# Performance work log

Hardware: AMD Instinct MI355X
Metric: run time of the kernel (lower is better)

Reference implementation:

```python
import jax, jax.numpy as jnp
import numpy as np

N_NODES = 100000
N_EDGES = 1600000
IN_DIM = 128
HID = 256
N_CLS = 32
BN_EPS = 1e-5


def _sage_conv(x, src, dst, Wl, bl, Wr, n_nodes):
    # PyG SAGEConv (mean aggr): out = lin_l(mean_{j->i} x_j) + lin_r(x_i)
    msgs = x[src]                                              # [E, D] gather
    agg = jax.ops.segment_sum(msgs, dst, num_segments=n_nodes)  # [N, D]
    deg = jax.ops.segment_sum(jnp.ones((src.shape[0],), x.dtype), dst,
                              num_segments=n_nodes)
    agg = agg / jnp.maximum(deg, 1.0)[:, None]                 # mean
    return agg @ Wl + bl + x @ Wr


def _batch_norm(x, gamma, beta):
    mu = jnp.mean(x, axis=0)
    var = jnp.var(x, axis=0)
    return (x - mu) * jax.lax.rsqrt(var + BN_EPS) * gamma + beta


def setup_inputs() -> dict:
    key = jax.random.key(0)
    ks = jax.random.split(key, 8)
    s = lambda d: 1.0 / np.sqrt(d)
    return {
        "x": jax.random.normal(ks[0], (N_NODES, IN_DIM), jnp.float32),
        "edge_src": jax.random.randint(ks[1], (N_EDGES,), 0, N_NODES),
        "edge_dst": jax.random.randint(ks[2], (N_EDGES,), 0, N_NODES),
        "W1l": jax.random.normal(ks[3], (IN_DIM, HID), jnp.float32) * s(IN_DIM),
        "b1": jnp.zeros((HID,), jnp.float32),
        "W1r": jax.random.normal(ks[4], (IN_DIM, HID), jnp.float32) * s(IN_DIM),
        "g1": jnp.ones((HID,), jnp.float32),
        "be1": jnp.zeros((HID,), jnp.float32),
        "W2l": jax.random.normal(ks[5], (HID, HID), jnp.float32) * s(HID),
        "b2": jnp.zeros((HID,), jnp.float32),
        "W2r": jax.random.normal(ks[6], (HID, HID), jnp.float32) * s(HID),
        "g2": jnp.ones((HID,), jnp.float32),
        "be2": jnp.zeros((HID,), jnp.float32),
        "Wfc": jax.random.normal(ks[7], (HID, N_CLS), jnp.float32) * s(HID),
        "bfc": jnp.zeros((N_CLS,), jnp.float32),
    }


def reference(x, edge_src, edge_dst, W1l, b1, W1r, g1, be1,
              W2l, b2, W2r, g2, be2, Wfc, bfc):
    n = x.shape[0]
    h = _sage_conv(x, edge_src, edge_dst, W1l, b1, W1r, n)
    h = jax.nn.relu(_batch_norm(h, g1, be1))
    # dropout is identity in deterministic/eval mode
    h = _sage_conv(h, edge_src, edge_dst, W2l, b2, W2r, n)
    h = jax.nn.relu(_batch_norm(h, g2, be2))
    return h @ Wfc + bfc
```

## Files before the change

### kernel.cpp

```cpp
#include <hip/hip_runtime.h>

#define N_NODES 100000
#define N_EDGES 1600000
#define IN_DIM 128
#define HID 256
#define N_CLS 32
#define BN_EPS 1e-5f

#define SCAN_CHUNK 1024
#define SCAN_NB ((N_NODES + SCAN_CHUNK - 1) / SCAN_CHUNK)
#define GEMM_NBY ((N_NODES + 127) / 128)
#define GEMM_NB (GEMM_NBY * 2)

#define NBUCK 16
#define BUCK_NODES 6250
#define BUCK_CAP 112000
#define PASSA_CHUNK 4096
#define PASSA_NB ((N_EDGES + PASSA_CHUNK - 1) / PASSA_CHUNK)
#define FILL_SUBS 64

typedef unsigned short bf16;
typedef __attribute__((ext_vector_type(8))) short short8;
typedef __attribute__((ext_vector_type(4))) float float4v;
typedef __attribute__((ext_vector_type(2))) float floatx2;

__device__ __forceinline__ float bf2f(bf16 h) {
    return __uint_as_float(((unsigned int)h) << 16);
}
__device__ __forceinline__ bf16 f2bf(float f) {
    unsigned int u = __float_as_uint(f);
    u += 0x7FFFu + ((u >> 16) & 1u);
    return (bf16)(u >> 16);
}
__device__ __forceinline__ float blo(unsigned int u) { return __uint_as_float(u << 16); }
__device__ __forceinline__ float bhi(unsigned int u) { return __uint_as_float(u & 0xFFFF0000u); }
__device__ __forceinline__ unsigned int pack2(float lo, float hi) {
    return (unsigned int)f2bf(lo) | ((unsigned int)f2bf(hi) << 16);
}

__device__ __forceinline__ void acc8_fp8(uint2 w, float* a) {
    floatx2 f0 = __builtin_amdgcn_cvt_pk_f32_fp8(w.x, false);
    floatx2 f1 = __builtin_amdgcn_cvt_pk_f32_fp8(w.x, true);
    floatx2 f2 = __builtin_amdgcn_cvt_pk_f32_fp8(w.y, false);
    floatx2 f3 = __builtin_amdgcn_cvt_pk_f32_fp8(w.y, true);
    a[0] += f0.x; a[1] += f0.y; a[2] += f1.x; a[3] += f1.y;
    a[4] += f2.x; a[5] += f2.y; a[6] += f3.x; a[7] += f3.y;
}
__device__ __forceinline__ unsigned int pack4_fp8(float a, float b, float c, float d) {
    int p = 0;
    p = __builtin_amdgcn_cvt_pk_fp8_f32(a, b, p, false);
    p = __builtin_amdgcn_cvt_pk_fp8_f32(c, d, p, true);
    return (unsigned int)p;
}

__device__ __forceinline__ void gload16(const void* g, void* l) {
    __builtin_amdgcn_global_load_lds(
        (const __attribute__((address_space(1))) void*)g,
        (__attribute__((address_space(3))) void*)l, 16, 0, 0);
}


__global__ __launch_bounds__(256) void bucket_scatter_kernel(
    const int* __restrict__ esrc, const int* __restrict__ edst,
    int* __restrict__ counts, int* __restrict__ bcur, int2* __restrict__ bstore) {
    __shared__ int lhist[NBUCK], lbase[NBUCK], gbase[NBUCK], lcur[NBUCK];
    __shared__ int2 stage[PASSA_CHUNK];
    const int tid = threadIdx.x;
    if (tid < NBUCK) lhist[tid] = 0;
    __syncthreads();

    const int base = blockIdx.x * PASSA_CHUNK;
    const int nedge = min(PASSA_CHUNK, N_EDGES - base);
    const bool act = (tid * 16) < nedge;
    int s[16], d[16], bk[16];
    if (act) {
        const int4* s4 = (const int4*)(esrc + base + tid * 16);
        const int4* d4 = (const int4*)(edst + base + tid * 16);
#pragma unroll
        for (int t = 0; t < 4; ++t) {
            int4 sv = s4[t], dv = d4[t];
            s[t * 4 + 0] = sv.x; s[t * 4 + 1] = sv.y; s[t * 4 + 2] = sv.z; s[t * 4 + 3] = sv.w;
            d[t * 4 + 0] = dv.x; d[t * 4 + 1] = dv.y; d[t * 4 + 2] = dv.z; d[t * 4 + 3] = dv.w;
        }
#pragma unroll
        for (int u = 0; u < 16; ++u) {
            bk[u] = (int)((unsigned)d[u] / BUCK_NODES);
            atomicAdd(&counts[d[u]], 1);
            atomicAdd(&lhist[bk[u]], 1);
        }
    }
    __syncthreads();
    if (tid == 0) {
        int run = 0;
#pragma unroll
        for (int b = 0; b < NBUCK; ++b) { lbase[b] = run; lcur[b] = run; run += lhist[b]; }
    }
    if (tid < NBUCK) gbase[tid] = atomicAdd(&bcur[tid], lhist[tid]);
    __syncthreads();
    if (act) {
#pragma unroll
        for (int u = 0; u < 16; ++u) {
            int p = atomicAdd(&lcur[bk[u]], 1);
            stage[p] = make_int2(s[u], d[u]);
        }
    }
    __syncthreads();
    for (int p = tid; p < nedge; p += 256) {
        int2 e = stage[p];
        int b = (int)((unsigned)e.y / BUCK_NODES);
        int gp = gbase[b] + (p - lbase[b]);
        if (gp < BUCK_CAP) bstore[(size_t)b * BUCK_CAP + gp] = e;
    }
}


__global__ __launch_bounds__(256) void fill_bucket_kernel(
    const int2* __restrict__ bstore, const int* __restrict__ bcnt,
    const int* __restrict__ off, int* __restrict__ cursor, int* __restrict__ csr) {
    const int bk = blockIdx.x & (NBUCK - 1);
    const int sub = blockIdx.x >> 4;
    const int n = bcnt[bk];
    const int2* ep = bstore + (size_t)bk * BUCK_CAP;
    for (int i = sub * 256 + threadIdx.x; i < n; i += 256 * FILL_SUBS) {
        int2 e = ep[i];
        int p = atomicAdd(&cursor[e.y], 1);
        csr[off[e.y] + p] = e.x;
    }
}


__global__ void scan1_kernel(const int* __restrict__ counts, int* __restrict__ bsums) {
    __shared__ int wsum[4];
    int base = blockIdx.x * SCAN_CHUNK + threadIdx.x * 4;
    int s = 0;
    if (base + 4 <= N_NODES) {
        int4 v = *(const int4*)(counts + base);
        s = v.x + v.y + v.z + v.w;
    } else {
        for (int j = 0; j < 4; ++j) if (base + j < N_NODES) s += counts[base + j];
    }
    for (int d = 32; d > 0; d >>= 1) s += __shfl_down(s, d, 64);
    if ((threadIdx.x & 63) == 0) wsum[threadIdx.x >> 6] = s;
    __syncthreads();
    if (threadIdx.x == 0) bsums[blockIdx.x] = wsum[0] + wsum[1] + wsum[2] + wsum[3];
}

__global__ void scan2_kernel(const int* __restrict__ bsums, int* __restrict__ boffs) {
    __shared__ int sh[128];
    int i = threadIdx.x;
    int v = (i < SCAN_NB) ? bsums[i] : 0;
    sh[i] = v;
    __syncthreads();
    for (int d = 1; d < 128; d <<= 1) {
        int t = (i >= d) ? sh[i - d] : 0;
        __syncthreads();
        sh[i] += t;
        __syncthreads();
    }
    if (i < SCAN_NB) boffs[i] = sh[i] - v;
}

__global__ void scan3_kernel(const int* __restrict__ counts, const int* __restrict__ boffs,
                             int* __restrict__ off) {
    __shared__ int sh[256];
    int tid = threadIdx.x;
    int base = blockIdx.x * SCAN_CHUNK + tid * 4;
    int c0 = 0, c1 = 0, c2 = 0, c3 = 0;
    if (base + 4 <= N_NODES) {
        int4 v = *(const int4*)(counts + base);
        c0 = v.x; c1 = v.y; c2 = v.z; c3 = v.w;
    } else {
        if (base + 0 < N_NODES) c0 = counts[base + 0];
        if (base + 1 < N_NODES) c1 = counts[base + 1];
        if (base + 2 < N_NODES) c2 = counts[base + 2];
        if (base + 3 < N_NODES) c3 = counts[base + 3];
    }
    int ts = c0 + c1 + c2 + c3;
    sh[tid] = ts;
    __syncthreads();
    for (int d = 1; d < 256; d <<= 1) {
        int t = (tid >= d) ? sh[tid - d] : 0;
        __syncthreads();
        sh[tid] += t;
        __syncthreads();
    }
    int run = boffs[blockIdx.x] + sh[tid] - ts;
    if (base + 0 < N_NODES) off[base + 0] = run; run += c0;
    if (base + 1 < N_NODES) off[base + 1] = run; run += c1;
    if (base + 2 < N_NODES) off[base + 2] = run; run += c2;
    if (base + 3 < N_NODES) off[base + 3] = run;
    if (blockIdx.x == 0 && tid == 0) off[N_NODES] = N_EDGES;
}


__global__ void convert_x_kernel(const float* __restrict__ x, bf16* __restrict__ xb,
                                 unsigned char* __restrict__ xf8) {
    int i = blockIdx.x * blockDim.x + threadIdx.x;
    int total4 = N_NODES * IN_DIM / 4;
    if (i >= total4) return;
    float4 v = ((const float4*)x)[i];
    ushort4 r;
    r.x = f2bf(v.x); r.y = f2bf(v.y); r.z = f2bf(v.z); r.w = f2bf(v.w);
    ((ushort4*)xb)[i] = r;
    ((unsigned int*)xf8)[i] = pack4_fp8(v.x, v.y, v.z, v.w);
}


__global__ void prep_weights_kernel(const float* __restrict__ W1l, const float* __restrict__ W1r,
                                    const float* __restrict__ W2l, const float* __restrict__ W2r,
                                    const float* __restrict__ Wfc,
                                    bf16* __restrict__ w1lt, bf16* __restrict__ w1rt,
                                    bf16* __restrict__ w2lt, bf16* __restrict__ w2rt,
                                    bf16* __restrict__ wfct) {
    const int S1 = IN_DIM * HID;
    const int S2 = HID * HID;
    const int S3 = HID * N_CLS;
    int i = blockIdx.x * blockDim.x + threadIdx.x;
    if (i < 2 * S1 + 2 * S2) {
        const float* W; bf16* Wt; int K, idx;
        if (i < S1)          { W = W1l; Wt = w1lt; K = IN_DIM; idx = i; }
        else if (i < 2 * S1) { W = W1r; Wt = w1rt; K = IN_DIM; idx = i - S1; }
        else if (i < 2 * S1 + S2) { W = W2l; Wt = w2lt; K = HID; idx = i - 2 * S1; }
        else                 { W = W2r; Wt = w2rt; K = HID; idx = i - 2 * S1 - S2; }
        int k = idx / HID, n = idx - k * HID;
        Wt[(size_t)n * K + k] = f2bf(W[idx]);
    } else if (i < 2 * S1 + 2 * S2 + S3) {
        int idx = i - 2 * S1 - 2 * S2;
        int k = idx >> 5, n = idx & 31;
        wfct[(size_t)n * HID + k] = f2bf(Wfc[idx]);
    }
}


__global__ void aggregate1_kernel(const unsigned char* __restrict__ xf8, const int* __restrict__ off,
                                  const int* __restrict__ csr, bf16* __restrict__ out) {
    int t = blockIdx.x * blockDim.x + threadIdx.x;
    int node = t >> 4;
    int sl = t & 15;
    if (node >= N_NODES) return;
    int s = off[node], e = off[node + 1];
    float inv = 1.0f / (float)max(e - s, 1);
    const uint2* f = (const uint2*)xf8;
    float a[8] = {0.f, 0.f, 0.f, 0.f, 0.f, 0.f, 0.f, 0.f};
    int i = s;
    for (; i + 4 <= e; i += 4) {
        int u0 = csr[i], u1 = csr[i + 1], u2 = csr[i + 2], u3 = csr[i + 3];
        uint2 w0 = f[(size_t)u0 * 16 + sl];
        uint2 w1 = f[(size_t)u1 * 16 + sl];
        uint2 w2 = f[(size_t)u2 * 16 + sl];
        uint2 w3 = f[(size_t)u3 * 16 + sl];
        acc8_fp8(w0, a); acc8_fp8(w1, a); acc8_fp8(w2, a); acc8_fp8(w3, a);
    }
    for (; i < e; ++i) {
        uint2 w = f[(size_t)csr[i] * 16 + sl];
        acc8_fp8(w, a);
    }
    uint4 r;
    r.x = pack2(a[0] * inv, a[1] * inv);
    r.y = pack2(a[2] * inv, a[3] * inv);
    r.z = pack2(a[4] * inv, a[5] * inv);
    r.w = pack2(a[6] * inv, a[7] * inv);
    ((uint4*)out)[(size_t)node * 16 + sl] = r;
}

__global__ void aggregate2_kernel(const unsigned char* __restrict__ hf8, const int* __restrict__ off,
                                  const int* __restrict__ csr, bf16* __restrict__ out) {
    int t = blockIdx.x * blockDim.x + threadIdx.x;
    int node = t >> 5;
    int sl = t & 31;
    if (node >= N_NODES) return;
    int s = off[node], e = off[node + 1];
    float inv = 1.0f / (float)max(e - s, 1);
    const uint2* f = (const uint2*)hf8;
    float a[8] = {0.f, 0.f, 0.f, 0.f, 0.f, 0.f, 0.f, 0.f};
    int i = s;
    for (; i + 4 <= e; i += 4) {
        int u0 = csr[i], u1 = csr[i + 1], u2 = csr[i + 2], u3 = csr[i + 3];
        uint2 w0 = f[(size_t)u0 * 32 + sl];
        uint2 w1 = f[(size_t)u1 * 32 + sl];
        uint2 w2 = f[(size_t)u2 * 32 + sl];
        uint2 w3 = f[(size_t)u3 * 32 + sl];
        acc8_fp8(w0, a); acc8_fp8(w1, a); acc8_fp8(w2, a); acc8_fp8(w3, a);
    }
    for (; i < e; ++i) {
        uint2 w = f[(size_t)csr[i] * 32 + sl];
        acc8_fp8(w, a);
    }
    uint4 r;
    r.x = pack2(a[0] * inv, a[1] * inv);
    r.y = pack2(a[2] * inv, a[3] * inv);
    r.z = pack2(a[4] * inv, a[5] * inv);
    r.w = pack2(a[6] * inv, a[7] * inv);
    ((uint4*)out)[(size_t)node * 32 + sl] = r;
}


#define AT_SZ 4096

__device__ __forceinline__ void stage_tile(
    const bf16* __restrict__ Ap, const bf16* __restrict__ Wp, int K, int k0,
    int tile_m, int tile_n, int M, int wave, int lane,
    bf16* bufA, bf16* bufW) {
#pragma unroll
    for (int is = 0; is < 2; ++is) {
        int lin = (wave * 2 + is) * 1024 + lane * 16;
        int row = lin >> 6;
        int seg = (lin >> 4) & 3;
        int ga = min(tile_m + row, M - 1);
        gload16(Ap + (size_t)ga * K + k0 + seg * 8, (char*)bufA + (wave * 2 + is) * 1024);
        gload16(Wp + (size_t)(tile_n + row) * K + k0 + seg * 8, (char*)bufW + (wave * 2 + is) * 1024);
    }
}

__global__ __launch_bounds__(256) void gemm_dual_mfma(
    const bf16* __restrict__ A, const bf16* __restrict__ WtA, int KA,
    const bf16* __restrict__ Bm, const bf16* __restrict__ WtB, int KB,
    const float* __restrict__ bias, bf16* __restrict__ C, int M,
    float* __restrict__ psum, float* __restrict__ psq) {
    __shared__ bf16 As[3 * AT_SZ];
    __shared__ bf16 Ws[3 * AT_SZ];
    __shared__ float sred[4][64];
    __shared__ float qred[4][64];
    const int tid = threadIdx.x;
    const int lane = tid & 63;
    const int wave = tid >> 6;
    const int rw = (wave >> 1) * 64;
    const int cw = (wave & 1) * 64;
    const int lrow = lane & 15;
    const int quad = lane >> 4;
    const int tile_m = blockIdx.y * 128;
    const int tile_n = blockIdx.x * 128;

    float4v acc[4][4];
#pragma unroll
    for (int i = 0; i < 4; ++i)
#pragma unroll
        for (int j = 0; j < 4; ++j) acc[i][j] = (float4v){0.f, 0.f, 0.f, 0.f};

    const int NTA = KA >> 5;
    const int NT = NTA + (KB >> 5);
    auto tsrc = [&](int t, const bf16*& Ap, const bf16*& Wp, int& K, int& k0) {
        if (t < NTA) { Ap = A;  Wp = WtA; K = KA; k0 = t << 5; }
        else         { Ap = Bm; Wp = WtB; K = KB; k0 = (t - NTA) << 5; }
    };

#pragma unroll
    for (int t = 0; t < 2; ++t) {
        const bf16 *Ap, *Wp; int K, k0; tsrc(t, Ap, Wp, K, k0);
        stage_tile(Ap, Wp, K, k0, tile_m, tile_n, M, wave, lane,
                   As + t * AT_SZ, Ws + t * AT_SZ);
    }

    for (int t = 0; t < NT; ++t) {
        if (t + 2 < NT) {
            const bf16 *Ap, *Wp; int K, k0; tsrc(t + 2, Ap, Wp, K, k0);
            int b = (t + 2) % 3;
            stage_tile(Ap, Wp, K, k0, tile_m, tile_n, M, wave, lane,
                       As + b * AT_SZ, Ws + b * AT_SZ);
        }
        if (t + 2 < NT)      asm volatile("s_waitcnt vmcnt(8)" ::: "memory");
        else if (t + 1 < NT) asm volatile("s_waitcnt vmcnt(4)" ::: "memory");
        else                 asm volatile("s_waitcnt vmcnt(0)" ::: "memory");
        __builtin_amdgcn_s_barrier();
        asm volatile("" ::: "memory");

        const bf16* bA = As + (t % 3) * AT_SZ;
        const bf16* bW = Ws + (t % 3) * AT_SZ;
        short8 a[4], b[4];
#pragma unroll
        for (int i = 0; i < 4; ++i)
            a[i] = *(const short8*)(bA + (rw + i * 16 + lrow) * 32 + quad * 8);
#pragma unroll
        for (int j = 0; j < 4; ++j)
            b[j] = *(const short8*)(bW + (cw + j * 16 + lrow) * 32 + quad * 8);
#pragma unroll
        for (int i = 0; i < 4; ++i)
#pragma unroll
            for (int j = 0; j < 4; ++j)
                acc[i][j] = __builtin_amdgcn_mfma_f32_16x16x32_bf16(a[i], b[j], acc[i][j], 0, 0, 0);

        asm volatile("" ::: "memory");
        __builtin_amdgcn_s_barrier();
    }

    bf16* slice = As + wave * 1024;
    float bvj[4];
#pragma unroll
    for (int j = 0; j < 4; ++j) bvj[j] = bias[tile_n + cw + j * 16 + lrow];
    float cs[4] = {0.f, 0.f, 0.f, 0.f}, cq[4] = {0.f, 0.f, 0.f, 0.f};

#pragma unroll
    for (int i = 0; i < 4; ++i) {
#pragma unroll
        for (int j = 0; j < 4; ++j) {
#pragma unroll
            for (int r = 0; r < 4; ++r) {
                int row = tile_m + rw + i * 16 + quad * 4 + r;
                float v = acc[i][j][r] + bvj[j];
                if (row < M) { cs[j] += v; cq[j] += v * v; }
                slice[(quad * 4 + r) * 64 + ((j ^ quad) * 16) + lrow] = f2bf(v);
            }
        }
        __syncthreads();
#pragma unroll
        for (int c = 0; c < 2; ++c) {
            int ch = lane + c * 64;
            int lr = ch >> 3, sg = ch & 7;
            int grow = tile_m + rw + i * 16 + lr;
            if (grow < M) {
                const bf16* srcp = slice + lr * 64 + (((sg >> 1) ^ (lr >> 2)) << 4) + ((sg & 1) << 3);
                uint4 v = *(const uint4*)srcp;
                *(uint4*)(C + (size_t)grow * HID + tile_n + cw + sg * 8) = v;
            }
        }
        __syncthreads();
    }

#pragma unroll
    for (int j = 0; j < 4; ++j) {
        cs[j] += __shfl_xor(cs[j], 16, 64); cs[j] += __shfl_xor(cs[j], 32, 64);
        cq[j] += __shfl_xor(cq[j], 16, 64); cq[j] += __shfl_xor(cq[j], 32, 64);
    }
    if (quad == 0) {
#pragma unroll
        for (int j = 0; j < 4; ++j) {
            sred[wave][j * 16 + lrow] = cs[j];
            qred[wave][j * 16 + lrow] = cq[j];
        }
    }
    __syncthreads();
    int bid = blockIdx.y * gridDim.x + blockIdx.x;
    if (tid < 128) {
        int grp = tid >> 6, idx = tid & 63;
        psum[(size_t)bid * 128 + tid] = sred[grp][idx] + sred[grp + 2][idx];
    } else {
        int t = tid - 128;
        int grp = t >> 6, idx = t & 63;
        psq[(size_t)bid * 128 + t] = qred[grp][idx] + qred[grp + 2][idx];
    }
}

__global__ void bn_finalize_kernel(const float* __restrict__ psum, const float* __restrict__ psq,
                                   float* __restrict__ stats, int nby) {
    const float* src = blockIdx.y ? psq : psum;
    int c = threadIdx.x;
    int bx = c >> 7, cl = c & 127;
    int per = (nby + gridDim.x - 1) / gridDim.x;
    int b0 = blockIdx.x * per, b1 = min(b0 + per, nby);
    float s = 0.f;
    for (int by = b0; by < b1; ++by) s += src[(size_t)(by * 2 + bx) * 128 + cl];
    atomicAdd(&stats[blockIdx.y * HID + c], s);
}


__global__ void bn_apply_relu_kernel(bf16* __restrict__ h, unsigned char* __restrict__ hf8,
                                     const float* __restrict__ stats,
                                     const float* __restrict__ g, const float* __restrict__ be,
                                     int M) {
    int i4 = blockIdx.x * blockDim.x + threadIdx.x;
    int total4 = M * (HID / 4);
    if (i4 >= total4) return;
    int col4 = i4 & (HID / 4 - 1);
    ushort4 v = ((const ushort4*)h)[i4];
    float invN = 1.0f / (float)M;
    float o[4] = {bf2f(v.x), bf2f(v.y), bf2f(v.z), bf2f(v.w)};
#pragma unroll
    for (int j = 0; j < 4; ++j) {
        int col = col4 * 4 + j;
        float mu = stats[col] * invN;
        float var = stats[HID + col] * invN - mu * mu;
        float sc = rsqrtf(var + BN_EPS) * g[col];
        float val = (o[j] - mu) * sc + be[col];
        o[j] = val > 0.f ? val : 0.f;
    }
    ushort4 r;
    r.x = f2bf(o[0]); r.y = f2bf(o[1]); r.z = f2bf(o[2]); r.w = f2bf(o[3]);
    ((ushort4*)h)[i4] = r;
    ((unsigned int*)hf8)[i4] = pack4_fp8(o[0], o[1], o[2], o[3]);
}


#define BSTR 264

__global__ __launch_bounds__(256) void fc_bn_mfma_kernel(
    const bf16* __restrict__ h, const float* __restrict__ stats,
    const float* __restrict__ g, const float* __restrict__ be,
    const bf16* __restrict__ WfcT, const float* __restrict__ bfc,
    float* __restrict__ out, int M) {
    __shared__ bf16 Bs[32 * BSTR];
    __shared__ float sc_s[HID], sh_s[HID];
    int tid = threadIdx.x;
    for (int i = tid; i < 32 * 32; i += 256) {
        int rrow = i >> 5, seg = i & 31;
        *(uint4*)(Bs + rrow * BSTR + seg * 8) = *(const uint4*)(WfcT + (size_t)rrow * HID + seg * 8);
    }
    {
        float invN = 1.0f / (float)M;
        float mu = stats[tid] * invN;
        float var = stats[HID + tid] * invN - mu * mu;
        float s = rsqrtf(var + BN_EPS) * g[tid];
        sc_s[tid] = s;
        sh_s[tid] = be[tid] - mu * s;
    }
    __syncthreads();
    int wave = tid >> 6, lane = tid & 63, lrow = lane & 15, quad = lane >> 4;
    int row = blockIdx.x * 64 + wave * 16 + lrow;
    const bf16* hrow = h + (size_t)row * HID;
    float4v acc0 = {0.f, 0.f, 0.f, 0.f}, acc1 = {0.f, 0.f, 0.f, 0.f};
#pragma unroll
    for (int ks = 0; ks < 8; ++ks) {
        int k0 = ks * 32 + quad * 8;
        uint4 av = {0u, 0u, 0u, 0u};
        if (row < M) av = *(const uint4*)(hrow + k0);
        union { unsigned int u[4]; short8 s8; } cvt;
        unsigned int* avp = (unsigned int*)&av;
#pragma unroll
        for (int t = 0; t < 4; ++t) {
            int k = k0 + t * 2;
            float v0 = blo(avp[t]) * sc_s[k] + sh_s[k];
            float v1 = bhi(avp[t]) * sc_s[k + 1] + sh_s[k + 1];
            v0 = v0 > 0.f ? v0 : 0.f;
            v1 = v1 > 0.f ? v1 : 0.f;
            cvt.u[t] = pack2(v0, v1);
        }
        short8 b0 = *(const short8*)(Bs + lrow * BSTR + k0);
        short8 b1 = *(const short8*)(Bs + (16 + lrow) * BSTR + k0);
        acc0 = __builtin_amdgcn_mfma_f32_16x16x32_bf16(cvt.s8, b0, acc0, 0, 0, 0);
        acc1 = __builtin_amdgcn_mfma_f32_16x16x32_bf16(cvt.s8, b1, acc1, 0, 0, 0);
    }
    int orow = blockIdx.x * 64 + wave * 16 + quad * 4;
    float bv0 = bfc[lrow], bv1 = bfc[16 + lrow];
#pragma unroll
    for (int r = 0; r < 4; ++r) {
        int rr = orow + r;
        if (rr < M) {
            out[(size_t)rr * N_CLS + lrow] = acc0[r] + bv0;
            out[(size_t)rr * N_CLS + 16 + lrow] = acc1[r] + bv1;
        }
    }
}


extern "C" void kernel_launch(void* const* d_in, const int* in_sizes, int n_in,
                              void* d_out, int out_size, void* d_ws, size_t ws_size,
                              hipStream_t stream) {
    const float* x   = (const float*)d_in[0];
    const int* esrc  = (const int*)d_in[1];
    const int* edst  = (const int*)d_in[2];
    const float* W1l = (const float*)d_in[3];
    const float* b1  = (const float*)d_in[4];
    const float* W1r = (const float*)d_in[5];
    const float* g1  = (const float*)d_in[6];
    const float* be1 = (const float*)d_in[7];
    const float* W2l = (const float*)d_in[8];
    const float* b2  = (const float*)d_in[9];
    const float* W2r = (const float*)d_in[10];
    const float* g2  = (const float*)d_in[11];
    const float* be2 = (const float*)d_in[12];
    const float* Wfc = (const float*)d_in[13];
    const float* bfc = (const float*)d_in[14];
    float* out = (float*)d_out;

    char* ws = (char*)d_ws;
    size_t o = 0;
    auto carve = [&](size_t bytes) {
        char* p = ws + o;
        o = (o + bytes + 255) & ~(size_t)255;
        return p;
    };
    int*   off    = (int*)carve((N_NODES + 1) * sizeof(int));
    int*   cursor = (int*)carve(N_NODES * sizeof(int));
    int*   csr    = (int*)carve(N_EDGES * sizeof(int));
    int*   bsums  = (int*)carve(SCAN_NB * sizeof(int));
    int*   boffs  = (int*)carve(SCAN_NB * sizeof(int));
    int*   bcur   = (int*)carve(NBUCK * sizeof(int));
    float* stats1 = (float*)carve(2 * HID * sizeof(float));
    float* stats2 = (float*)carve(2 * HID * sizeof(float));
    float* psum   = (float*)carve((size_t)GEMM_NB * 128 * sizeof(float));
    float* psq    = (float*)carve((size_t)GEMM_NB * 128 * sizeof(float));
    bf16*  w1lt   = (bf16*)carve((size_t)IN_DIM * HID * sizeof(bf16));
    bf16*  w1rt   = (bf16*)carve((size_t)IN_DIM * HID * sizeof(bf16));
    bf16*  w2lt   = (bf16*)carve((size_t)HID * HID * sizeof(bf16));
    bf16*  w2rt   = (bf16*)carve((size_t)HID * HID * sizeof(bf16));
    bf16*  wfct   = (bf16*)carve((size_t)N_CLS * HID * sizeof(bf16));
    bf16*  agg    = (bf16*)carve((size_t)N_NODES * HID * sizeof(bf16));
    bf16*  h1     = (bf16*)carve((size_t)N_NODES * HID * sizeof(bf16));
    bf16*  h2     = (bf16*)carve((size_t)N_NODES * HID * sizeof(bf16));
    bf16*          xb   = h2;
    unsigned char* xf8  = (unsigned char*)h2 + (size_t)N_NODES * IN_DIM * sizeof(bf16);
    unsigned char* h1f8 = (unsigned char*)h2;
    int2*          bstore = (int2*)agg;

    if (o > ws_size) return;

    hipMemsetAsync(cursor, 0, N_NODES * sizeof(int), stream);
    hipMemsetAsync(bcur, 0, NBUCK * sizeof(int), stream);
    hipMemsetAsync(stats1, 0, 2 * HID * sizeof(float), stream);
    hipMemsetAsync(stats2, 0, 2 * HID * sizeof(float), stream);

    bucket_scatter_kernel<<<PASSA_NB, 256, 0, stream>>>(esrc, edst, cursor, bcur, bstore);
    scan1_kernel<<<SCAN_NB, 256, 0, stream>>>(cursor, bsums);
    scan2_kernel<<<1, 128, 0, stream>>>(bsums, boffs);
    scan3_kernel<<<SCAN_NB, 256, 0, stream>>>(cursor, boffs, off);
    hipMemsetAsync(cursor, 0, N_NODES * sizeof(int), stream);
    fill_bucket_kernel<<<NBUCK * FILL_SUBS, 256, 0, stream>>>(bstore, bcur, off, cursor, csr);

    convert_x_kernel<<<(N_NODES * IN_DIM / 4 + 255) / 256, 256, 0, stream>>>(x, xb, xf8);
    {
        int total = 2 * IN_DIM * HID + 2 * HID * HID + HID * N_CLS;
        prep_weights_kernel<<<(total + 255) / 256, 256, 0, stream>>>(
            W1l, W1r, W2l, W2r, Wfc, w1lt, w1rt, w2lt, w2rt, wfct);
    }

    const dim3 ggrid(HID / 128, GEMM_NBY);

    aggregate1_kernel<<<(N_NODES * 16 + 255) / 256, 256, 0, stream>>>(xf8, off, csr, agg);
    gemm_dual_mfma<<<ggrid, 256, 0, stream>>>(
        agg, w1lt, IN_DIM, xb, w1rt, IN_DIM, b1, h1, N_NODES, psum, psq);
    bn_finalize_kernel<<<dim3(8, 2), 256, 0, stream>>>(psum, psq, stats1, GEMM_NBY);
    {
        int total4 = N_NODES * (HID / 4);
        bn_apply_relu_kernel<<<(total4 + 255) / 256, 256, 0, stream>>>(h1, h1f8, stats1, g1, be1, N_NODES);
    }

    aggregate2_kernel<<<(N_NODES * 32 + 255) / 256, 256, 0, stream>>>(h1f8, off, csr, agg);
    gemm_dual_mfma<<<ggrid, 256, 0, stream>>>(
        agg, w2lt, HID, h1, w2rt, HID, b2, h2, N_NODES, psum, psq);
    bn_finalize_kernel<<<dim3(8, 2), 256, 0, stream>>>(psum, psq, stats2, GEMM_NBY);

    fc_bn_mfma_kernel<<<(N_NODES + 63) / 64, 256, 0, stream>>>(
        h2, stats2, g2, be2, wfct, bfc, out, N_NODES);
}
```

Measured before the change: 557.2 us.

## Replace global per-node degree atomics with LDS bucket histograms

The per-edge global atomicAdd on node degree counts is removed from the bucket scatter pass. A new kernel builds per-bucket degree histograms in shared memory over slices of each bucket, and writes partial counts that the first scan kernel sums into the final counts. The scatter chunk size is also halved to launch more blocks. This trades 1.6M scattered global atomics for an extra kernel launch plus about 6.4 MB of partial-count writes and reads.

```diff
diff --git a/kernel.cpp b/kernel.cpp
--- a/kernel.cpp
+++ b/kernel.cpp
@@ -15,9 +15,10 @@
 #define NBUCK 16
 #define BUCK_NODES 6250
 #define BUCK_CAP 112000
-#define PASSA_CHUNK 4096
+#define PASSA_CHUNK 2048
 #define PASSA_NB ((N_EDGES + PASSA_CHUNK - 1) / PASSA_CHUNK)
 #define FILL_SUBS 64
+#define HSUBS 16
 
 typedef unsigned short bf16;
 typedef __attribute__((ext_vector_type(8))) short short8;
@@ -62,7 +63,7 @@
 
 __global__ __launch_bounds__(256) void bucket_scatter_kernel(
     const int* __restrict__ esrc, const int* __restrict__ edst,
-    int* __restrict__ counts, int* __restrict__ bcur, int2* __restrict__ bstore) {
+    int* __restrict__ bcur, int2* __restrict__ bstore) {
     __shared__ int lhist[NBUCK], lbase[NBUCK], gbase[NBUCK], lcur[NBUCK];
     __shared__ int2 stage[PASSA_CHUNK];
     const int tid = threadIdx.x;
@@ -71,21 +72,20 @@
 
     const int base = blockIdx.x * PASSA_CHUNK;
     const int nedge = min(PASSA_CHUNK, N_EDGES - base);
-    const bool act = (tid * 16) < nedge;
-    int s[16], d[16], bk[16];
+    const bool act = (tid * 8) < nedge;
+    int s[8], d[8], bk[8];
     if (act) {
-        const int4* s4 = (const int4*)(esrc + base + tid * 16);
-        const int4* d4 = (const int4*)(edst + base + tid * 16);
-#pragma unroll
-        for (int t = 0; t < 4; ++t) {
+        const int4* s4 = (const int4*)(esrc + base + tid * 8);
+        const int4* d4 = (const int4*)(edst + base + tid * 8);
+#pragma unroll
+        for (int t = 0; t < 2; ++t) {
             int4 sv = s4[t], dv = d4[t];
             s[t * 4 + 0] = sv.x; s[t * 4 + 1] = sv.y; s[t * 4 + 2] = sv.z; s[t * 4 + 3] = sv.w;
             d[t * 4 + 0] = dv.x; d[t * 4 + 1] = dv.y; d[t * 4 + 2] = dv.z; d[t * 4 + 3] = dv.w;
         }
 #pragma unroll
-        for (int u = 0; u < 16; ++u) {
+        for (int u = 0; u < 8; ++u) {
             bk[u] = (int)((unsigned)d[u] / BUCK_NODES);
-            atomicAdd(&counts[d[u]], 1);
             atomicAdd(&lhist[bk[u]], 1);
         }
     }
@@ -99,7 +99,7 @@
     __syncthreads();
     if (act) {
 #pragma unroll
-        for (int u = 0; u < 16; ++u) {
+        for (int u = 0; u < 8; ++u) {
             int p = atomicAdd(&lcur[bk[u]], 1);
             stage[p] = make_int2(s[u], d[u]);
         }
@@ -111,6 +111,28 @@
         int gp = gbase[b] + (p - lbase[b]);
         if (gp < BUCK_CAP) bstore[(size_t)b * BUCK_CAP + gp] = e;
     }
+}
+
+
+__global__ __launch_bounds__(256) void bucket_hist_kernel(
+    const int2* __restrict__ bstore, const int* __restrict__ bcnt,
+    int* __restrict__ partial) {
+    __shared__ int hist[BUCK_NODES];
+    const int bk = blockIdx.x & (NBUCK - 1);
+    const int sl = blockIdx.x >> 4;
+    for (int i = threadIdx.x; i < BUCK_NODES; i += 256) hist[i] = 0;
+    __syncthreads();
+    const int n = bcnt[bk];
+    const int per = (n + HSUBS - 1) / HSUBS;
+    const int i0 = sl * per, i1 = min(i0 + per, n);
+    const int2* ep = bstore + (size_t)bk * BUCK_CAP;
+    const int nbase = bk * BUCK_NODES;
+    for (int i = i0 + threadIdx.x; i < i1; i += 256) {
+        atomicAdd(&hist[ep[i].y - nbase], 1);
+    }
+    __syncthreads();
+    int* dst = partial + (size_t)sl * N_NODES + nbase;
+    for (int i = threadIdx.x; i < BUCK_NODES; i += 256) dst[i] = hist[i];
 }
 
 
@@ -129,16 +151,30 @@
 }
 
 
-__global__ void scan1_kernel(const int* __restrict__ counts, int* __restrict__ bsums) {
+__global__ void scan1_kernel(const int* __restrict__ partial, int* __restrict__ counts,
+                             int* __restrict__ bsums) {
     __shared__ int wsum[4];
     int base = blockIdx.x * SCAN_CHUNK + threadIdx.x * 4;
-    int s = 0;
+    int c0 = 0, c1 = 0, c2 = 0, c3 = 0;
     if (base + 4 <= N_NODES) {
-        int4 v = *(const int4*)(counts + base);
-        s = v.x + v.y + v.z + v.w;
+#pragma unroll
+        for (int sl = 0; sl < HSUBS; ++sl) {
+            int4 v = *(const int4*)(partial + (size_t)sl * N_NODES + base);
+            c0 += v.x; c1 += v.y; c2 += v.z; c3 += v.w;
+        }
+        int4 w; w.x = c0; w.y = c1; w.z = c2; w.w = c3;
+        *(int4*)(counts + base) = w;
     } else {
-        for (int j = 0; j < 4; ++j) if (base + j < N_NODES) s += counts[base + j];
-    }
+        for (int j = 0; j < 4; ++j) {
+            if (base + j < N_NODES) {
+                int c = 0;
+                for (int sl = 0; sl < HSUBS; ++sl) c += partial[(size_t)sl * N_NODES + base + j];
+                counts[base + j] = c;
+                if (j == 0) c0 = c; else if (j == 1) c1 = c; else if (j == 2) c2 = c; else c3 = c;
+            }
+        }
+    }
+    int s = c0 + c1 + c2 + c3;
     for (int d = 32; d > 0; d >>= 1) s += __shfl_down(s, d, 64);
     if ((threadIdx.x & 63) == 0) wsum[threadIdx.x >> 6] = s;
     __syncthreads();
@@ -590,16 +626,17 @@
     unsigned char* xf8  = (unsigned char*)h2 + (size_t)N_NODES * IN_DIM * sizeof(bf16);
     unsigned char* h1f8 = (unsigned char*)h2;
     int2*          bstore = (int2*)agg;
+    int*           partial = (int*)h1;
 
     if (o > ws_size) return;
 
-    hipMemsetAsync(cursor, 0, N_NODES * sizeof(int), stream);
     hipMemsetAsync(bcur, 0, NBUCK * sizeof(int), stream);
     hipMemsetAsync(stats1, 0, 2 * HID * sizeof(float), stream);
     hipMemsetAsync(stats2, 0, 2 * HID * sizeof(float), stream);
 
-    bucket_scatter_kernel<<<PASSA_NB, 256, 0, stream>>>(esrc, edst, cursor, bcur, bstore);
-    scan1_kernel<<<SCAN_NB, 256, 0, stream>>>(cursor, bsums);
+    bucket_scatter_kernel<<<PASSA_NB, 256, 0, stream>>>(esrc, edst, bcur, bstore);
+    bucket_hist_kernel<<<NBUCK * HSUBS, 256, 0, stream>>>(bstore, bcur, partial);
+    scan1_kernel<<<SCAN_NB, 256, 0, stream>>>(partial, cursor, bsums);
     scan2_kernel<<<1, 128, 0, stream>>>(bsums, boffs);
     scan3_kernel<<<SCAN_NB, 256, 0, stream>>>(cursor, boffs, off);
     hipMemsetAsync(cursor, 0, N_NODES * sizeof(int), stream);
```

New measurement: 512.2 us. -8.1%, faster.
